# Kernel tuning notes

Measured on AMD Instinct MI355X. Metric: run time of the kernel, lower is better.

## Reference

```python
import jax, jax.numpy as jnp
import numpy as np

ALPHA = 0.1
B, T, D = 32, 1024, 384


def _build_alive(T):
    # Expert j (1-indexed) is created at time j with lifetime 2^(ctz(j)+2)+1.
    def lifetime(j):
        k = (j & -j).bit_length() - 1
        return 2 ** (k + 2) + 1

    sets = [[j for j in range(1, t + 1) if t < j + lifetime(j)]
            for t in range(1, T + 1)]
    K = max(len(s) for s in sets)
    # pad with sentinel index T (the extra never-consumed expert slot)
    idx = np.full((T, K), T, dtype=np.int32)
    mask = np.zeros((T, K), dtype=np.float32)
    for t0, s in enumerate(sets):
        for i, j in enumerate(s):
            idx[t0, i] = j - 1  # 0-indexed expert slot
            mask[t0, i] = 1.0
    return idx, mask


def setup_inputs() -> dict:
    key = jax.random.key(0)
    kx, kw, kb = jax.random.split(key, 3)
    n_exp = T + 1
    x = jax.random.normal(kx, (B, T, D), dtype=jnp.float32)
    # stand-in STULayer = Linear(D, D) per expert
    W = jax.random.normal(kw, (n_exp, D, D), dtype=jnp.float32) / np.float32(np.sqrt(D))
    b = jax.random.normal(kb, (n_exp, D), dtype=jnp.float32) * 0.02
    idx, mask = _build_alive(T)
    return {"x": x, "W": W, "b": b,
            "alive_idx": jnp.asarray(idx), "alive_mask": jnp.asarray(mask)}


def reference(x, W, b, alive_idx, alive_mask):
    Bb, Tt, Dd = x.shape
    n_exp = W.shape[0]
    # initial pool: 1 expert with weight 1
    p0 = jnp.zeros((n_exp,), x.dtype).at[0].set(1.0)
    new_idx = jnp.arange(1, Tt + 1, dtype=jnp.int32)      # slot of expert created at step t
    t_f = jnp.arange(1, Tt + 1, dtype=x.dtype)            # p[new] = 1/t

    def step(p, inp):
        x_t, idx, mask, ni, tf = inp          # x_t: [B,D]; idx,mask: [K]
        Wg = W[idx]                            # [K,D,D]
        bg = b[idx]                            # [K,D]
        outs = jnp.einsum('bd,kde->kbe', x_t, Wg) + bg[:, None, :]  # [K,B,D]
        p_a = p[idx] * mask                    # weights of alive experts
        w = p_a / jnp.sum(p_a)                 # normalized (torch keeps them pre-normalized)
        y_t = jnp.einsum('k,kbe->be', w, outs)
        # soft cross-entropy of expert outputs against x_t (ChunkedCrossEntropyLoss stand-in)
        tgt = jax.nn.softmax(x_t, axis=-1)                       # [B,D]
        logp = jax.nn.log_softmax(outs, axis=-1)                 # [K,B,D]
        loss = -jnp.mean(jnp.sum(tgt[None, :, :] * logp, axis=-1), axis=-1)  # [K]
        loss = jax.lax.stop_gradient(loss)     # torch uses .item() => detached
        # multiplicative weight update, normalize over alive set
        p_upd = p_a * jnp.exp(-ALPHA * loss) * mask
        p_upd = p_upd / jnp.sum(p_upd)
        p = p.at[idx].set(jnp.where(mask > 0, p_upd, p[idx]))
        # spawn new expert with weight 1/t (renormalization deferred to use time)
        p = p.at[ni].set(1.0 / tf)
        return p, y_t

    xs = (jnp.swapaxes(x, 0, 1), alive_idx, alive_mask, new_idx, t_f)
    _, ys = jax.lax.scan(step, p0, xs)        # ys: [T,B,D]
    return jnp.swapaxes(ys, 0, 1)
```

## Files before the change

### kernel.cpp

```cpp
#include <hip/hip_runtime.h>

#define TT 1024
#define BB 32
#define DD 384
#define NE 1025
#define ALPHA_ 0.1f
#define TC 4
#define KSTEP 64
#define NKS 6
#define MROWS 128
#define PADK 72
#define NTHR 512

typedef __attribute__((ext_vector_type(8))) short short8;
typedef __attribute__((ext_vector_type(8))) unsigned short ushort8;
typedef __attribute__((ext_vector_type(4))) float f32x4;

__device__ __forceinline__ unsigned short f2bf(float f) {
    unsigned int u = __float_as_uint(f);
    unsigned int r = u + 0x7fffu + ((u >> 16) & 1u);
    return (unsigned short)(r >> 16);
}

__device__ __host__ __forceinline__ int chunks_of(int j, int* Lout) {
    int k = __builtin_ctz(j);
    int life = (1 << (k + 2)) + 1;
    int jend = j + life - 1; if (jend > TT) jend = TT;
    int L = jend - j + 1;
    *Lout = L;
    return (L + TC - 1) / TC;
}

__device__ __forceinline__ void gl16(const void* g, void* l) {
    __builtin_amdgcn_global_load_lds(
        (const __attribute__((address_space(1))) void*)g,
        (__attribute__((address_space(3))) void*)l, 16, 0, 0);
}

__device__ __forceinline__ float dppsum32(float v) {
    float t;
    t = __int_as_float(__builtin_amdgcn_update_dpp(0, __float_as_int(v), 0x111, 0xf, 0xf, true)); v += t;
    t = __int_as_float(__builtin_amdgcn_update_dpp(0, __float_as_int(v), 0x112, 0xf, 0xf, true)); v += t;
    t = __int_as_float(__builtin_amdgcn_update_dpp(0, __float_as_int(v), 0x114, 0xf, 0xf, true)); v += t;
    t = __int_as_float(__builtin_amdgcn_update_dpp(0, __float_as_int(v), 0x118, 0xf, 0xf, true)); v += t;
    t = __int_as_float(__builtin_amdgcn_update_dpp(0, __float_as_int(v), 0x142, 0xf, 0xf, true)); v += t;
    return __int_as_float(__builtin_amdgcn_readlane(__float_as_int(v), 31));
}

__global__ void setup_all(int* __restrict__ table, int* __restrict__ pref,
                          short* __restrict__ perm16,
                          const int* __restrict__ aidx, const float* __restrict__ amask,
                          int K) {
    __shared__ int sc[1024];
    int b = blockIdx.x, t = threadIdx.x;
    if (b == 0) {
        int j = t + 1;
        int L; int nc = chunks_of(j, &L);
        int start = 0;
        for (int jp = 1; jp < j; ++jp) { int Lp; start += chunks_of(jp, &Lp); }
        for (int c = 0; c < nc; ++c) {
            int cnt = L - c * TC; if (cnt > TC) cnt = TC;
            int* e = table + 3 * (start + c);
            e[0] = j - 1;
            e[1] = (j - 1) + c * TC;
            e[2] = cnt;
        }
    } else if (b == 1) {
        int c = 0;
        for (int kk = 0; kk < K; ++kk) c += (amask[t * K + kk] > 0.f) ? 1 : 0;
        sc[t] = c;
        __syncthreads();
        for (int off = 1; off < 1024; off <<= 1) {
            int v = (t >= off) ? sc[t - off] : 0;
            __syncthreads();
            sc[t] += v;
            __syncthreads();
        }
        if (t == 0) pref[0] = 0;
        pref[t + 1] = sc[t];
    } else {
        int t0 = b - 2;
        int l = t;
        if (l < 32) {
            short enc = 63;
            if (t0 >= 1 && t0 <= TT - 1 && l < K && amask[t0 * K + l] > 0.f) {
                int sp = aidx[t0 * K + l];
                if (sp == t0) enc = (short)(-sp);
                else {
                    for (int kk = 0; kk < K; ++kk)
                        if (aidx[(t0 - 1) * K + kk] == sp) { enc = (short)kk; break; }
                }
            }
            perm16[t0 * 32 + l] = enc;
        }
    }
}

__global__ __launch_bounds__(512)
void conv_w2(const float* __restrict__ W, unsigned short* __restrict__ Wperm) {
    int db = blockIdx.x;
    int j  = blockIdx.y;
    int tid = threadIdx.x, l = tid & 63, w8 = tid >> 6;
    const float* Wj = W + (size_t)j * (DD * DD)
                        + (size_t)(db * 32 + (l >> 4) * 8) * DD + (l & 15);
#pragma unroll
    for (int it = 0; it < 3; ++it) {
        int eblk = it * 8 + w8;
        const float* src = Wj + eblk * 16;
        ushort8 h;
#pragma unroll
        for (int k = 0; k < 8; ++k) h[k] = f2bf(src[(size_t)k * DD]);
        *(ushort8*)&Wperm[(((size_t)j * 12 + db) * 24 + eblk) * 512 + l * 8] = h;
    }
}

__global__ __launch_bounds__(512)
void conv_x2(const float* __restrict__ x, unsigned short* __restrict__ xperm) {
    int t = blockIdx.x;
    int tid = threadIdx.x, l = tid & 63, w8 = tid >> 6;
#pragma unroll
    for (int it = 0; it < 3; ++it) {
        int T = it * 8 + w8;
        int bb = T / 12, db = T - bb * 12;
        const float* src = x + ((size_t)(bb * 16 + (l & 15)) * TT + t) * DD
                             + db * 32 + (l >> 4) * 8;
        float4 f0 = *(const float4*)src;
        float4 f1 = *(const float4*)(src + 4);
        ushort8 h;
        h[0] = f2bf(f0.x); h[1] = f2bf(f0.y); h[2] = f2bf(f0.z); h[3] = f2bf(f0.w);
        h[4] = f2bf(f1.x); h[5] = f2bf(f1.y); h[6] = f2bf(f1.z); h[7] = f2bf(f1.w);
        *(ushort8*)&xperm[(size_t)t * 12288 + T * 512 + l * 8] = h;
    }
}

__global__ void conv_tgt(const float* __restrict__ x, unsigned short* __restrict__ tgtbf) {
    __shared__ unsigned short sL[8 * 384];
    int tid = threadIdx.x;
    int wid = tid >> 6, lane = tid & 63;
    size_t row = (size_t)blockIdx.x * 8 + wid;
    const float* xr = x + row * DD;
    float v[6]; float m = -1e30f;
#pragma unroll
    for (int i = 0; i < 6; ++i) { v[i] = xr[lane + 64 * i]; m = fmaxf(m, v[i]); }
#pragma unroll
    for (int d = 1; d < 64; d <<= 1) m = fmaxf(m, __shfl_xor(m, d));
    float s = 0.f;
#pragma unroll
    for (int i = 0; i < 6; ++i) { v[i] = __expf(v[i] - m); s += v[i]; }
#pragma unroll
    for (int d = 1; d < 64; d <<= 1) s += __shfl_xor(s, d);
    float rz = 1.0f / s;
#pragma unroll
    for (int i = 0; i < 6; ++i) sL[wid * 384 + lane + 64 * i] = f2bf(v[i] * rz);
    __syncthreads();
    unsigned int* dst = (unsigned int*)(tgtbf + (size_t)blockIdx.x * 8 * 384);
    const unsigned int* s32 = (const unsigned int*)sL;
#pragma unroll
    for (int i = 0; i < 3; ++i) dst[i * 512 + tid] = s32[i * 512 + tid];
}

__global__ __launch_bounds__(1024)
void gemmA(const unsigned short* __restrict__ xperm,
           const unsigned short* __restrict__ Wperm,
           const float* __restrict__ bias,
           const int* __restrict__ aidx,
           const unsigned short* __restrict__ tgtbf,
           float* __restrict__ Epad,
           const int* __restrict__ table, int nblk, int K,
           const int* __restrict__ pref,
           unsigned short* __restrict__ outs)
{
    __shared__ __align__(16) unsigned short sA[2][4096];
    __shared__ __align__(16) unsigned short sB[2][12288];
    __shared__ float sRow[128];
    __shared__ int sKK[TC];
    __shared__ int sSlot[TC];

    int bid = blockIdx.x;
    int q8 = nblk >> 3, r8 = nblk & 7;
    int xcd = bid & 7, pos = bid >> 3;
    int lb = (xcd < r8 ? xcd * (q8 + 1) : r8 * (q8 + 1) + (xcd - r8) * q8) + pos;

    int s = table[3 * lb], t0s = table[3 * lb + 1], cnt = table[3 * lb + 2];

    int tid = threadIdx.x;
    int wid = tid >> 6, lane = tid & 63;
    int waveM = wid >> 2, waveN = wid & 3;
    int lc = lane & 15, lg = lane >> 4;

    int tcl[4];
#pragma unroll
    for (int tc = 0; tc < 4; ++tc) { int t = t0s + tc; tcl[tc] = t > TT - 1 ? TT - 1 : t; }

    f32x4 acc[2][6];
    f32x4 zz = {0.f, 0.f, 0.f, 0.f};
#pragma unroll
    for (int m = 0; m < 2; ++m)
#pragma unroll
        for (int n = 0; n < 6; ++n) acc[m][n] = zz;

    const size_t wbase = (size_t)s * (12 * 24 * 512);

    auto stage = [&](int buf, int ks) {
        if (wid < 8) {
            int tc = wid >> 1, bb = wid & 1;
            const unsigned short* asrc = xperm + ((size_t)tcl[tc] * 24 + bb * 12 + ks) * 512 + lane * 8;
            gl16(asrc, &sA[buf][wid * 512]);
            const unsigned short* bsrc = Wperm + wbase + ((size_t)ks * 24 + 16 + wid) * 512 + lane * 8;
            gl16(bsrc, &sB[buf][(16 + wid) * 512]);
        } else {
            int e0 = (wid - 8) * 2;
            const unsigned short* b0 = Wperm + wbase + ((size_t)ks * 24 + e0) * 512 + lane * 8;
            gl16(b0, &sB[buf][e0 * 512]);
            gl16(b0 + 512, &sB[buf][(e0 + 1) * 512]);
        }
    };

    stage(0, 0);
    stage(1, 1);
    for (int ks = 0; ks < 12; ++ks) {
        int cur = ks & 1;
        if (ks < 11) asm volatile("s_waitcnt vmcnt(2)" ::: "memory");
        else         asm volatile("s_waitcnt vmcnt(0)" ::: "memory");
        __builtin_amdgcn_s_barrier();
        __builtin_amdgcn_sched_barrier(0);
        short8 af[2], bfr[6];
#pragma unroll
        for (int mf = 0; mf < 2; ++mf)
            af[mf] = *(const short8*)&sA[cur][(waveM * 2 + mf) * 512 + lane * 8];
#pragma unroll
        for (int nf = 0; nf < 6; ++nf)
            bfr[nf] = *(const short8*)&sB[cur][(waveN * 6 + nf) * 512 + lane * 8];
#pragma unroll
        for (int mf = 0; mf < 2; ++mf)
#pragma unroll
            for (int nf = 0; nf < 6; ++nf)
                acc[mf][nf] = __builtin_amdgcn_mfma_f32_16x16x32_bf16(af[mf], bfr[nf], acc[mf][nf], 0, 0, 0);
        __builtin_amdgcn_sched_barrier(0);
        __builtin_amdgcn_s_barrier();
        __builtin_amdgcn_sched_barrier(0);
        if (ks < 10) stage(cur, ks + 2);
    }
    __syncthreads();

    float* sStat = (float*)&sA[0][0];
    if (tid < TC) {
        int kk = 0, slot = 0;
        if (tid < cnt) {
            int t = t0s + tid;
            for (int k2 = 0; k2 < K; ++k2)
                if (aidx[t * K + k2] == s) { kk = k2; break; }
            if (pref) slot = pref[t] + kk;
        }
        sKK[tid] = kk;
        sSlot[tid] = slot;
    }
#pragma unroll
    for (int nf = 0; nf < 6; ++nf) {
        float be = bias[(size_t)s * DD + waveN * 96 + nf * 16 + lc];
#pragma unroll
        for (int mf = 0; mf < 2; ++mf)
#pragma unroll
            for (int rr = 0; rr < 4; ++rr) acc[mf][nf][rr] += be;
    }
#pragma unroll
    for (int mf = 0; mf < 2; ++mf)
#pragma unroll
        for (int rr = 0; rr < 4; ++rr) {
            float m = acc[mf][0][rr];
#pragma unroll
            for (int nf = 1; nf < 6; ++nf) m = fmaxf(m, acc[mf][nf][rr]);
#pragma unroll
            for (int d = 1; d < 16; d <<= 1) m = fmaxf(m, __shfl_xor(m, d));
            if (lc == 0) sStat[(waveM * 32 + mf * 16 + lg * 4 + rr) * 12 + waveN] = m;
        }
    __syncthreads();
    if (outs && waveM < cnt) {
        unsigned short* ob = outs + (size_t)sSlot[waveM] * 12288;
#pragma unroll
        for (int mf = 0; mf < 2; ++mf)
#pragma unroll
            for (int nf = 0; nf < 6; ++nf) {
                int e = waveN * 96 + nf * 16 + lc;
#pragma unroll
                for (int rr = 0; rr < 4; ++rr) {
                    int b = mf * 16 + lg * 4 + rr;
                    ob[b * 384 + e] = f2bf(acc[mf][nf][rr]);
                }
            }
    }
#pragma unroll
    for (int mf = 0; mf < 2; ++mf)
#pragma unroll
        for (int rr = 0; rr < 4; ++rr) {
            int row = waveM * 32 + mf * 16 + lg * 4 + rr;
            const f32x4 pm = *(const f32x4*)&sStat[row * 12];
            float rmax = fmaxf(fmaxf(pm[0], pm[1]), fmaxf(pm[2], pm[3]));
            int tcr = row >> 5, b = row & 31;
            int t = tcl[tcr];
            const unsigned short* tg = tgtbf + ((size_t)b * TT + t) * DD;
            float psum = 0.f, pdot = 0.f;
#pragma unroll
            for (int nf = 0; nf < 6; ++nf) {
                int e = waveN * 96 + nf * 16 + lc;
                float a = acc[mf][nf][rr];
                psum += __expf(a - rmax);
                float tv = __uint_as_float(((unsigned int)tg[e]) << 16);
                pdot += tv * a;
            }
#pragma unroll
            for (int d = 1; d < 16; d <<= 1) { psum += __shfl_xor(psum, d); pdot += __shfl_xor(pdot, d); }
            if (lc == 0) { sStat[row * 12 + 4 + waveN] = psum; sStat[row * 12 + 8 + waveN] = pdot; }
        }
    __syncthreads();
    if (wid == 0) {
#pragma unroll
        for (int h = 0; h < 2; ++h) {
            int row = lane + h * 64;
            const f32x4 mm = *(const f32x4*)&sStat[row * 12];
            const f32x4 pp = *(const f32x4*)&sStat[row * 12 + 4];
            const f32x4 dd = *(const f32x4*)&sStat[row * 12 + 8];
            float rmax = fmaxf(fmaxf(mm[0], mm[1]), fmaxf(mm[2], mm[3]));
            float S = pp[0] + pp[1] + pp[2] + pp[3];
            float Dt = dd[0] + dd[1] + dd[2] + dd[3];
            sRow[row] = rmax + logf(S) - Dt;
        }
    }
    __syncthreads();
    if (wid == 0) {
#pragma unroll
        for (int pph = 0; pph < 2; ++pph) {
            int tc = pph * 2 + (lane >> 5);
            int b = lane & 31;
            float v = (tc < cnt) ? sRow[tc * 32 + b] : 0.f;
#pragma unroll
            for (int d = 1; d < 32; d <<= 1) v += __shfl_xor(v, d);
            if (b == 0 && tc < cnt) {
                float loss = v * (1.0f / 32.0f);
                float E = expf(-ALPHA_ * loss);
                int t0 = t0s + tc;
                Epad[t0 * 32 + sKK[tc]] = E;
            }
        }
    }
}

__global__ __launch_bounds__(256)
void recur3(const float* __restrict__ Epad, const short* __restrict__ perm16,
            const int* __restrict__ aidx, const float* __restrict__ amask,
            float* __restrict__ wraw, int K) {
    __shared__ __align__(16) float sE[2][4096];
    __shared__ __align__(16) short sP[2][4160];
    int tid = threadIdx.x, wid = tid >> 6, lane = tid & 63;
    int l = lane;

    auto stageCh = [&](int buf, int c) {
        const float* eb = Epad + c * 4096;
#pragma unroll
        for (int i = wid; i < 16; i += 4)
            gl16(eb + i * 256 + lane * 4, &sE[buf][i * 256]);
        const short* pb = perm16 + (c * 128 + 1) * 32;
#pragma unroll
        for (int i = wid; i < 8; i += 4)
            gl16(pb + i * 512 + lane * 8, &sP[buf][32 + i * 512]);
    };

    stageCh(0, 0);
    __syncthreads();

    float pr = 0.f;
    if (l < K && amask[l] > 0.f && aidx[l] == 0) pr = 1.f;

    int buf = 0;
    for (int c = 0; c < 8; ++c) {
        if (c < 7) stageCh(buf ^ 1, c + 1);
        if (wid == 0) {
            float curE = (l < 32) ? sE[buf][l] : 0.f;
            short curP = (l < 32) ? sP[buf][32 + l] : (short)63;
            for (int tl = 0; tl < 128; ++tl) {
                float nE = 0.f; short nP = 63;
                if (tl < 127) {
                    nE = sE[buf][(tl + 1) * 32 + (l & 31)];
                    nP = sP[buf][(tl + 2) * 32 + (l & 31)];
                }
                int t = c * 128 + tl;
                if (l < 32) wraw[t * 32 + l] = pr;
                float qv = pr * curE;
                float S2 = dppsum32(qv);
                float pn = qv / S2;
                int pe = (l < 32) ? (int)curP : 63;
                int src = pe >= 0 ? pe : 0;
                float sv = __shfl(pn, src);
                pr = (pe >= 0) ? sv : (1.0f / (float)(-pe));
                curE = (l < 32) ? nE : 0.f;
                curP = nP;
            }
        }
        __syncthreads();
        buf ^= 1;
    }
}

__global__ void wnorm(float* __restrict__ w) {
    int tid = threadIdx.x;
    int wid = tid >> 6, lane = tid & 63;
    int half = lane >> 5, l = lane & 31;
    int t = blockIdx.x * 8 + wid * 2 + half;
    float v = w[t * 32 + l];
    float s = v;
#pragma unroll
    for (int d = 1; d < 32; d <<= 1) s += __shfl_xor(s, d);
    w[t * 32 + l] = v / s;
}

__global__ __launch_bounds__(512)
void mixout(const unsigned short* __restrict__ outs, const float* __restrict__ wts32,
            const int* __restrict__ pref, float* __restrict__ y) {
    int t = blockIdx.x;
    __shared__ float sW[32];
    int tid = threadIdx.x;
    if (tid < 32) sW[tid] = wts32[t * 32 + tid];
    __syncthreads();
    int p0 = pref[t];
    int L = pref[t + 1] - p0;
    float acc[24];
#pragma unroll
    for (int i = 0; i < 24; ++i) acc[i] = 0.f;
    const ushort8* base = (const ushort8*)(outs + (size_t)p0 * 12288);
    for (int kk = 0; kk < L; ++kk) {
        float w = sW[kk];
        const ushort8* sp = base + (size_t)kk * 1536;
#pragma unroll
        for (int pass = 0; pass < 3; ++pass) {
            ushort8 v = sp[pass * 512 + tid];
#pragma unroll
            for (int j = 0; j < 8; ++j)
                acc[pass * 8 + j] += w * __uint_as_float(((unsigned int)v[j]) << 16);
        }
    }
#pragma unroll
    for (int pass = 0; pass < 3; ++pass) {
        int c = pass * 512 + tid;
        int b = c / 48;
        int e = (c % 48) * 8;
        float* yr = y + ((size_t)b * TT + t) * DD + e;
        float4 f0, f1;
        f0.x = acc[pass * 8 + 0]; f0.y = acc[pass * 8 + 1];
        f0.z = acc[pass * 8 + 2]; f0.w = acc[pass * 8 + 3];
        f1.x = acc[pass * 8 + 4]; f1.y = acc[pass * 8 + 5];
        f1.z = acc[pass * 8 + 6]; f1.w = acc[pass * 8 + 7];
        *(float4*)yr = f0;
        *(float4*)(yr + 4) = f1;
    }
}

__global__ void setup_blocks(int* __restrict__ table) {
    int j = threadIdx.x + 1;
    int L; int nc = chunks_of(j, &L);
    int start = 0;
    for (int jp = 1; jp < j; ++jp) { int Lp; start += chunks_of(jp, &Lp); }
    for (int c = 0; c < nc; ++c) {
        int cnt = L - c * TC; if (cnt > TC) cnt = TC;
        int* e = table + 3 * (start + c);
        e[0] = j - 1;
        e[1] = (j - 1) + c * TC;
        e[2] = cnt;
    }
}

__global__ void setup_union(int* __restrict__ uCount, int* __restrict__ uList) {
    int c = threadIdx.x;
    int t1 = 2 * c + 1, t2 = 2 * c + 2;
    int n = 0;
    for (int j = 1; j <= t2 && j <= TT; ++j) {
        int k = __builtin_ctz(j);
        int life = (1 << (k + 2)) + 1;
        if (j + life - 1 >= t1) { if (n < 32) uList[c * 32 + n] = j - 1; n++; }
    }
    uCount[c] = n > 32 ? 32 : n;
}

__global__ void setup_perm3(const int* __restrict__ aidx, const float* __restrict__ amask,
                            short* __restrict__ perm16, int K) {
    int t0 = blockIdx.x;
    int l = threadIdx.x;
    short enc = 63;
    if (t0 >= 1 && t0 <= TT - 1 && l < K && amask[t0 * K + l] > 0.f) {
        int sp = aidx[t0 * K + l];
        if (sp == t0) enc = (short)(-sp);
        else {
            for (int kk = 0; kk < K; ++kk)
                if (aidx[(t0 - 1) * K + kk] == sp) { enc = (short)kk; break; }
        }
    }
    perm16[t0 * 32 + l] = enc;
}

__global__ void conv_w(const float* __restrict__ W, unsigned short* __restrict__ Wperm) {
    int db = blockIdx.x;
    int j  = blockIdx.y;
    __shared__ __align__(16) unsigned short sL[12288];
    int tid = threadIdx.x;
    int r = tid >> 4, q = tid & 15;
    const float* src = W + (size_t)j * (DD * DD) + (size_t)(db * 32 + r) * DD + q * 24;
#pragma unroll
    for (int i = 0; i < 6; ++i) {
        float4 f = *(const float4*)(src + i * 4);
        int e0 = q * 24 + i * 4;
        float fv[4] = {f.x, f.y, f.z, f.w};
#pragma unroll
        for (int m = 0; m < 4; ++m) {
            int e = e0 + m;
            int off = (e >> 4) * 512 + (r >> 3) * 128 + (e & 15) * 8 + (r & 7);
            sL[off] = f2bf(fv[m]);
        }
    }
    __syncthreads();
    ushort8* dst = (ushort8*)(Wperm + ((size_t)j * 12 + db) * 12288);
    const ushort8* s8 = (const ushort8*)sL;
#pragma unroll
    for (int i = 0; i < 3; ++i) dst[tid * 3 + i] = s8[tid * 3 + i];
}

__global__ void conv_x(const float* __restrict__ x, unsigned short* __restrict__ xperm) {
    int t = blockIdx.x;
    __shared__ __align__(16) unsigned short sL[12288];
    int tid = threadIdx.x;
    int b = tid >> 4, q = tid & 15;
    const float* src = x + ((size_t)b * TT + t) * DD + q * 24;
#pragma unroll
    for (int i = 0; i < 6; ++i) {
        float4 f = *(const float4*)(src + i * 4);
        int d0 = q * 24 + i * 4;
        float fv[4] = {f.x, f.y, f.z, f.w};
#pragma unroll
        for (int m = 0; m < 4; ++m) {
            int d = d0 + m;
            int off = ((b >> 4) * 12 + (d >> 5)) * 512 + ((d >> 3) & 3) * 128 + (b & 15) * 8 + (d & 7);
            sL[off] = f2bf(fv[m]);
        }
    }
    __syncthreads();
    ushort8* dst = (ushort8*)(xperm + (size_t)t * 12288);
    const ushort8* s8 = (const ushort8*)sL;
#pragma unroll
    for (int i = 0; i < 3; ++i) dst[tid * 3 + i] = s8[tid * 3 + i];
}

__global__ __launch_bounds__(1024)
void gemmC(const unsigned short* __restrict__ xperm,
           const unsigned short* __restrict__ Wperm,
           const float* __restrict__ bias,
           const int* __restrict__ aidx,
           const float* __restrict__ wts32,
           const int* __restrict__ uCount, const int* __restrict__ uList,
           float* __restrict__ y, int K)
{
    __shared__ __align__(16) unsigned short sAF[24576];
    __shared__ __align__(16) unsigned short sB[2][12288];
    __shared__ float sWu[64];
    __shared__ int   sUL[32];
    __shared__ float sBv[768];

    int nb = gridDim.x;
    int bid = blockIdx.x;
    int q8 = nb >> 3, r8 = nb & 7;
    int xcd = bid & 7, pos = bid >> 3;
    int c = (xcd < r8 ? xcd * (q8 + 1) : r8 * (q8 + 1) + (xcd - r8) * q8) + pos;

    int t0 = c * 2;
    int tid = threadIdx.x, wid = tid >> 6, lane = tid & 63;
    int waveM = wid >> 2, waveN = wid & 3;
    int lc = lane & 15, lg = lane >> 4;
    int tcw = waveM >> 1, bbw = waveM & 1;

    int uc = uCount[c];
    if (tid < uc) sUL[tid] = uList[c * 32 + tid];
#pragma unroll
    for (int i = 0; i < 3; ++i) {
        int T = wid * 3 + i;
        int tc = T / 24, bb = (T / 12) & 1, db = T % 12;
        const unsigned short* src = xperm + ((size_t)(t0 + tc) * 24 + bb * 12 + db) * 512 + lane * 8;
        gl16(src, &sAF[T * 512]);
    }
    __syncthreads();
    if (tid < 2 * uc) {
        int u = tid >> 1, tc = tid & 1;
        int j = sUL[u];
        float wv = 0.f;
        for (int kk = 0; kk < K; ++kk)
            if (aidx[(t0 + tc) * K + kk] == j) { wv = wts32[(t0 + tc) * 32 + kk]; break; }
        sWu[u * 2 + tc] = wv;
    }
    __syncthreads();
    {
        size_t wb = (size_t)sUL[0] * (12 * 24 * 512);
        const unsigned short* b0 = Wperm + wb + (size_t)wid * 512 + lane * 8;
        gl16(b0, &sB[0][wid * 512]);
        if (wid < 8) {
            const unsigned short* b1 = Wperm + wb + (size_t)(16 + wid) * 512 + lane * 8;
            gl16(b1, &sB[0][(16 + wid) * 512]);
        }
    }
    for (int i = tid; i < 768; i += 1024) {
        int tc = (i >= 384) ? 1 : 0; int e = i - tc * 384;
        float a = 0.f;
        for (int u = 0; u < uc; ++u) a += sWu[u * 2 + tc] * bias[(size_t)sUL[u] * DD + e];
        sBv[i] = a;
    }
    __syncthreads();

    f32x4 accY[6], accE[6];
    f32x4 zz = {0.f, 0.f, 0.f, 0.f};
#pragma unroll
    for (int n = 0; n < 6; ++n) { accY[n] = zz; accE[n] = zz; }

    int buf = 0;
    for (int u = 0; u < uc; ++u) {
        float wv = sWu[u * 2 + tcw];
        bool act = (wv != 0.f);
        for (int ks = 0; ks < 12; ++ks) {
            int nu = u, nk = ks + 1;
            if (nk == 12) { nk = 0; nu = u + 1; }
            if (nu < uc) {
                size_t wb = (size_t)sUL[nu] * (12 * 24 * 512) + (size_t)nk * (24 * 512);
                const unsigned short* b0 = Wperm + wb + (size_t)wid * 512 + lane * 8;
                gl16(b0, &sB[buf ^ 1][wid * 512]);
                if (wid < 8) {
                    const unsigned short* b1 = Wperm + wb + (size_t)(16 + wid) * 512 + lane * 8;
                    gl16(b1, &sB[buf ^ 1][(16 + wid) * 512]);
                }
            }
            if (act) {
                short8 af = *(const short8*)&sAF[(waveM * 12 + ks) * 512 + lane * 8];
#pragma unroll
                for (int nf = 0; nf < 6; ++nf) {
                    short8 bf = *(const short8*)&sB[buf][(waveN * 6 + nf) * 512 + lane * 8];
                    accE[nf] = __builtin_amdgcn_mfma_f32_16x16x32_bf16(af, bf, accE[nf], 0, 0, 0);
                }
            }
            __syncthreads();
            buf ^= 1;
        }
        if (act) {
#pragma unroll
            for (int nf = 0; nf < 6; ++nf)
#pragma unroll
                for (int rr = 0; rr < 4; ++rr) { accY[nf][rr] += wv * accE[nf][rr]; accE[nf][rr] = 0.f; }
        }
    }

    int t = t0 + tcw;
#pragma unroll
    for (int nf = 0; nf < 6; ++nf) {
        int e = waveN * 96 + nf * 16 + lc;
        float bvv = sBv[tcw * 384 + e];
#pragma unroll
        for (int rr = 0; rr < 4; ++rr) {
            int b = bbw * 16 + lg * 4 + rr;
            y[((size_t)b * TT + t) * DD + e] = accY[nf][rr] + bvv;
        }
    }
}

__global__ void rowstats(const float* __restrict__ x, float* __restrict__ xm,
                         float* __restrict__ rz) {
    int wid = threadIdx.x >> 6;
    int lane = threadIdx.x & 63;
    int row = blockIdx.x * 4 + wid;
    const float* xr = x + (size_t)row * DD;
    float v[6];
    float m = -1e30f;
#pragma unroll
    for (int i = 0; i < 6; ++i) { v[i] = xr[lane + 64 * i]; m = fmaxf(m, v[i]); }
#pragma unroll
    for (int d = 1; d < 64; d <<= 1) m = fmaxf(m, __shfl_xor(m, d));
    float s = 0.f;
#pragma unroll
    for (int i = 0; i < 6; ++i) s += expf(v[i] - m);
#pragma unroll
    for (int d = 1; d < 64; d <<= 1) s += __shfl_xor(s, d);
    if (lane == 0) { xm[row] = m; rz[row] = 1.0f / s; }
}

template<int MODE>
__global__ __launch_bounds__(NTHR)
void gemm_phase(const float* __restrict__ x, const float* __restrict__ W,
                const float* __restrict__ bias, const int* __restrict__ aidx,
                const float* __restrict__ xm, const float* __restrict__ rz,
                const float* __restrict__ wts, float* __restrict__ Earr,
                float* __restrict__ y, const int* __restrict__ table,
                int nblk, int K)
{
    __shared__ __align__(16) unsigned short sA[MROWS * PADK];
    __shared__ __align__(16) unsigned short sB[DD * PADK];
    __shared__ float sRow[MROWS];
    __shared__ float sCoef[TC];

    int bid = blockIdx.x;
    int q = nblk >> 3, r = nblk & 7;
    int xcd = bid & 7, pos = bid >> 3;
    int lb = (xcd < r ? xcd * (q + 1) : r * (q + 1) + (xcd - r) * q) + pos;

    int s = table[3 * lb], t0s = table[3 * lb + 1], cnt = table[3 * lb + 2];

    int tid = threadIdx.x;
    int wid = tid >> 6, lane = tid & 63;
    int waveM = wid >> 2, waveN = wid & 3;
    int lc = lane & 15, lg = lane >> 4;

    if (MODE == 1 && tid < TC) {
        float c = 0.f;
        if (tid < cnt) {
            int t0 = t0s + tid;
            for (int kk = 0; kk < K; ++kk)
                if (aidx[t0 * K + kk] == s) { c = wts[t0 * K + kk]; break; }
        }
        sCoef[tid] = c;
    }

    f32x4 acc[4][6];
    f32x4 zz = {0.f, 0.f, 0.f, 0.f};
#pragma unroll
    for (int i = 0; i < 4; ++i)
#pragma unroll
        for (int n = 0; n < 6; ++n) acc[i][n] = zz;

    const float* Wj = W + (size_t)s * (DD * DD);

    int xr = tid >> 2, xq = tid & 3;
    int xtc = xr >> 5, xb = xr & 31;
    int xt = t0s + xtc; if (xt > TT - 1) xt = TT - 1;
    const float* xrow = x + ((size_t)xb * TT + xt) * DD;

    for (int ks = 0; ks < NKS; ++ks) {
        const int d0 = ks * KSTEP;
        __syncthreads();
        {
            const float4* src = (const float4*)(xrow + d0 + xq * 16);
            float4 f0 = src[0], f1 = src[1], f2 = src[2], f3 = src[3];
            short8 v0, v1;
            v0[0] = (short)f2bf(f0.x); v0[1] = (short)f2bf(f0.y);
            v0[2] = (short)f2bf(f0.z); v0[3] = (short)f2bf(f0.w);
            v0[4] = (short)f2bf(f1.x); v0[5] = (short)f2bf(f1.y);
            v0[6] = (short)f2bf(f1.z); v0[7] = (short)f2bf(f1.w);
            v1[0] = (short)f2bf(f2.x); v1[1] = (short)f2bf(f2.y);
            v1[2] = (short)f2bf(f2.z); v1[3] = (short)f2bf(f2.w);
            v1[4] = (short)f2bf(f3.x); v1[5] = (short)f2bf(f3.y);
            v1[6] = (short)f2bf(f3.z); v1[7] = (short)f2bf(f3.w);
            short8* dst = (short8*)&sA[xr * PADK + xq * 16];
            dst[0] = v0; dst[1] = v1;
        }
        {
            int dbase = d0 + wid * 8;
#pragma unroll
            for (int g = 0; g < 6; ++g) {
                int e = g * 64 + lane;
                const float* col = Wj + (size_t)dbase * DD + e;
                short8 h;
#pragma unroll
                for (int dd = 0; dd < 8; ++dd) h[dd] = (short)f2bf(col[(size_t)dd * DD]);
                *(short8*)&sB[e * PADK + wid * 8] = h;
            }
        }
        __syncthreads();
#pragma unroll
        for (int kh = 0; kh < 2; ++kh) {
            short8 af[4], bfr[6];
#pragma unroll
            for (int mf = 0; mf < 4; ++mf)
                af[mf] = *(const short8*)&sA[(waveM * 64 + mf * 16 + lc) * PADK + kh * 32 + lg * 8];
#pragma unroll
            for (int nf = 0; nf < 6; ++nf)
                bfr[nf] = *(const short8*)&sB[(waveN * 96 + nf * 16 + lc) * PADK + kh * 32 + lg * 8];
#pragma unroll
            for (int mf = 0; mf < 4; ++mf)
#pragma unroll
                for (int nf = 0; nf < 6; ++nf)
                    acc[mf][nf] = __builtin_amdgcn_mfma_f32_16x16x32_bf16(af[mf], bfr[nf], acc[mf][nf], 0, 0, 0);
        }
    }

    if (MODE == 0) {
        __syncthreads();
        float* sStat = (float*)sA;
#pragma unroll
        for (int nf = 0; nf < 6; ++nf) {
            float be = bias[(size_t)s * DD + waveN * 96 + nf * 16 + lc];
#pragma unroll
            for (int mf = 0; mf < 4; ++mf)
#pragma unroll
                for (int rr = 0; rr < 4; ++rr) acc[mf][nf][rr] += be;
        }
#pragma unroll
        for (int mf = 0; mf < 4; ++mf)
#pragma unroll
            for (int rr = 0; rr < 4; ++rr) {
                float m = acc[mf][0][rr];
#pragma unroll
                for (int nf = 1; nf < 6; ++nf) m = fmaxf(m, acc[mf][nf][rr]);
#pragma unroll
                for (int d = 1; d < 16; d <<= 1) m = fmaxf(m, __shfl_xor(m, d));
                if (lc == 0) sStat[(waveM * 64 + mf * 16 + lg * 4 + rr) * 12 + waveN] = m;
            }
        __syncthreads();
#pragma unroll
        for (int mf = 0; mf < 4; ++mf)
#pragma unroll
            for (int rr = 0; rr < 4; ++rr) {
                int row = waveM * 64 + mf * 16 + lg * 4 + rr;
                const f32x4 pm = *(const f32x4*)&sStat[row * 12];
                float rmax = fmaxf(fmaxf(pm[0], pm[1]), fmaxf(pm[2], pm[3]));
                int tc = row >> 5, b = row & 31;
                int t = t0s + tc; if (t > TT - 1) t = TT - 1;
                float xmv = xm[b * TT + t];
                float rzv = rz[b * TT + t];
                const float* x2 = x + ((size_t)b * TT + t) * DD;
                float psum = 0.f, pdot = 0.f;
#pragma unroll
                for (int nf = 0; nf < 6; ++nf) {
                    int e = waveN * 96 + nf * 16 + lc;
                    float a = acc[mf][nf][rr];
                    psum += __expf(a - rmax);
                    float tg = __expf(x2[e] - xmv) * rzv;
                    pdot += tg * a;
                }
#pragma unroll
                for (int d = 1; d < 16; d <<= 1) {
                    psum += __shfl_xor(psum, d);
                    pdot += __shfl_xor(pdot, d);
                }
                if (lc == 0) { sStat[row * 12 + 4 + waveN] = psum; sStat[row * 12 + 8 + waveN] = pdot; }
            }
        __syncthreads();
        if (wid == 0) {
#pragma unroll
            for (int h = 0; h < 2; ++h) {
                int row = lane + h * 64;
                const f32x4 mm = *(const f32x4*)&sStat[row * 12];
                const f32x4 pp = *(const f32x4*)&sStat[row * 12 + 4];
                const f32x4 dd = *(const f32x4*)&sStat[row * 12 + 8];
                float rmax = fmaxf(fmaxf(mm[0], mm[1]), fmaxf(mm[2], mm[3]));
                float S = pp[0] + pp[1] + pp[2] + pp[3];
                float Dt = dd[0] + dd[1] + dd[2] + dd[3];
                sRow[row] = rmax + logf(S) - Dt;
            }
        }
        __syncthreads();
        if (wid == 0) {
#pragma unroll
            for (int pph = 0; pph < 2; ++pph) {
                int tc = pph * 2 + (lane >> 5);
                int b = lane & 31;
                float v = (tc < cnt) ? sRow[tc * 32 + b] : 0.f;
#pragma unroll
                for (int d = 1; d < 32; d <<= 1) v += __shfl_xor(v, d);
                if (b == 0 && tc < cnt) {
                    float loss = v * (1.0f / 32.0f);
                    float E = expf(-ALPHA_ * loss);
                    int t0 = t0s + tc;
                    for (int kk = 0; kk < K; ++kk)
                        if (aidx[t0 * K + kk] == s) { Earr[t0 * K + kk] = E; break; }
                }
            }
        }
    } else {
#pragma unroll
        for (int mf = 0; mf < 4; ++mf)
#pragma unroll
            for (int rr = 0; rr < 4; ++rr) {
                int row = waveM * 64 + mf * 16 + lg * 4 + rr;
                int tc = row >> 5, b = row & 31;
                if (tc < cnt) {
                    float c = sCoef[tc];
                    int t = t0s + tc;
                    float* yr = y + ((size_t)b * TT + t) * DD + waveN * 96 + lc;
#pragma unroll
                    for (int nf = 0; nf < 6; ++nf)
                        atomicAdd(yr + nf * 16, c * acc[mf][nf][rr]);
                }
            }
    }
}

__global__ void recurrence(const int* __restrict__ aidx, const float* __restrict__ amask,
                           const float* __restrict__ Earr, float* __restrict__ wts, int K) {
    __shared__ float p[NE];
    int l = threadIdx.x;
    for (int i = l; i < NE; i += 64) p[i] = 0.f;
    __syncthreads();
    if (l == 0) p[0] = 1.f;
    __syncthreads();

    int idxv = TT; float mv = 0.f, Ev = 1.f;
    if (l < K) { idxv = aidx[l]; mv = amask[l]; Ev = Earr[l]; }

    for (int t0 = 0; t0 < TT; ++t0) {
        int idxn = TT; float mn = 0.f, En = 1.f;
        if (t0 + 1 < TT && l < K) {
            idxn = aidx[(t0 + 1) * K + l];
            mn = amask[(t0 + 1) * K + l];
            En = Earr[(t0 + 1) * K + l];
        }
        float pa = (l < K) ? p[idxv] * mv : 0.f;
        float qv = pa * Ev;
        float S1 = pa, S2 = qv;
#pragma unroll
        for (int d = 1; d < 64; d <<= 1) {
            S1 += __shfl_xor(S1, d);
            S2 += __shfl_xor(S2, d);
        }
        float w = pa / S1;
        if (l < K) wts[t0 * K + l] = w;
        float pn = qv / S2;
        __syncthreads();
        if (l < K && mv > 0.f) p[idxv] = pn;
        if (l == 0) p[t0 + 1] = 1.0f / (float)(t0 + 1);
        __syncthreads();
        idxv = idxn; mv = mn; Ev = En;
    }
}

__global__ void bias_init(const float* __restrict__ bias, const int* __restrict__ aidx,
                          const float* __restrict__ wts, float* __restrict__ y, int K) {
    int t0 = blockIdx.x;
    int e = threadIdx.x;
    float acc = 0.f;
    for (int kk = 0; kk < K; ++kk) {
        float w = wts[t0 * K + kk];
        int s = aidx[t0 * K + kk];
        acc += w * bias[(size_t)s * DD + e];
    }
    for (int b = 0; b < BB; ++b)
        y[((size_t)b * TT + t0) * DD + e] = acc;
}

extern "C" void kernel_launch(void* const* d_in, const int* in_sizes, int n_in,
                              void* d_out, int out_size, void* d_ws, size_t ws_size,
                              hipStream_t stream) {
    const float* x = (const float*)d_in[0];
    const float* W = (const float*)d_in[1];
    const float* bv = (const float*)d_in[2];
    const int* aidx = (const int*)d_in[3];
    const float* amask = (const float*)d_in[4];
    float* y = (float*)d_out;
    const int K = in_sizes[3] / TT;

    int nblk = 0, NSLOT = 0;
    for (int j = 1; j <= TT; ++j) { int L; nblk += chunks_of(j, &L); NSLOT += L; }

    size_t szW = (size_t)1024 * 294912;
    size_t szX = (size_t)1024 * 24576;
    size_t szT = (size_t)BB * TT * DD * 2;
    size_t szEp = (size_t)TT * 32 * sizeof(float);
    size_t szWt = (size_t)TT * 32 * sizeof(float);
    size_t szPm = (size_t)(TT + 1) * 32 * sizeof(short);
    size_t szTab = (size_t)6144 * 3 * sizeof(int);
    size_t szUC = 512 * sizeof(int);
    size_t szUL = 512 * 32 * sizeof(int);
    size_t szO  = (size_t)NSLOT * 12288 * 2;
    size_t szPf = (size_t)(TT + 1) * sizeof(int);
    size_t need2 = szW + szX + szT + szEp + szWt + szPm + szTab + szUC + szUL + 256;
    size_t need1 = need2 + szO + szPf;

    if (ws_size >= need1) {
        unsigned char* p = (unsigned char*)d_ws;
        unsigned short* Wperm = (unsigned short*)p; p += szW;
        unsigned short* xperm = (unsigned short*)p; p += szX;
        unsigned short* tgtb  = (unsigned short*)p; p += szT;
        float* Epad = (float*)p; p += szEp;
        float* wts32 = (float*)p; p += szWt;
        short* perm16 = (short*)p; p += szPm;
        int* table  = (int*)p;   p += szTab;
        int* uCnt   = (int*)p;   p += szUC;
        int* uLst   = (int*)p;   p += szUL;
        int* pref   = (int*)p;   p += szPf;
        unsigned short* outs = (unsigned short*)p; p += szO;

        hipLaunchKernelGGL(setup_all, dim3(TT + 3), dim3(1024), 0, stream,
                           table, pref, perm16, aidx, amask, K);
        hipLaunchKernelGGL(conv_w2, dim3(12, 1024), dim3(512), 0, stream, W, Wperm);
        hipLaunchKernelGGL(conv_x2, dim3(TT), dim3(512), 0, stream, x, xperm);
        hipLaunchKernelGGL(conv_tgt, dim3(BB * TT / 8), dim3(512), 0, stream, x, tgtb);
        hipMemsetAsync(Epad, 0, szEp, stream);
        hipLaunchKernelGGL(gemmA, dim3(nblk), dim3(1024), 0, stream,
                           xperm, Wperm, bv, aidx, tgtb, Epad, table, nblk, K, pref, outs);
        hipLaunchKernelGGL(recur3, dim3(1), dim3(256), 0, stream,
                           Epad, perm16, aidx, amask, wts32, K);
        hipLaunchKernelGGL(wnorm, dim3(TT / 8), dim3(256), 0, stream, wts32);
        hipLaunchKernelGGL(mixout, dim3(TT), dim3(512), 0, stream, outs, wts32, pref, y);
    } else if (ws_size >= need2) {
        unsigned char* p = (unsigned char*)d_ws;
        unsigned short* Wperm = (unsigned short*)p; p += szW;
        unsigned short* xperm = (unsigned short*)p; p += szX;
        unsigned short* tgtb  = (unsigned short*)p; p += szT;
        float* Epad = (float*)p; p += szEp;
        float* wts32 = (float*)p; p += szWt;
        short* perm16 = (short*)p; p += szPm;
        int* table  = (int*)p;   p += szTab;
        int* uCnt   = (int*)p;   p += szUC;
        int* uLst   = (int*)p;   p += szUL;

        hipLaunchKernelGGL(setup_blocks, dim3(1), dim3(1024), 0, stream, table);
        hipLaunchKernelGGL(setup_union, dim3(1), dim3(512), 0, stream, uCnt, uLst);
        hipLaunchKernelGGL(setup_perm3, dim3(TT + 1), dim3(32), 0, stream, aidx, amask, perm16, K);
        hipLaunchKernelGGL(conv_w, dim3(12, 1024), dim3(512), 0, stream, W, Wperm);
        hipLaunchKernelGGL(conv_x, dim3(TT), dim3(512), 0, stream, x, xperm);
        hipLaunchKernelGGL(conv_tgt, dim3(BB * TT / 8), dim3(512), 0, stream, x, tgtb);
        hipMemsetAsync(Epad, 0, szEp, stream);
        hipLaunchKernelGGL(gemmA, dim3(nblk), dim3(1024), 0, stream,
                           xperm, Wperm, bv, aidx, tgtb, Epad, table, nblk, K,
                           (const int*)nullptr, (unsigned short*)nullptr);
        hipLaunchKernelGGL(recur3, dim3(1), dim3(256), 0, stream,
                           Epad, perm16, aidx, amask, wts32, K);
        hipLaunchKernelGGL(wnorm, dim3(TT / 8), dim3(256), 0, stream, wts32);
        hipLaunchKernelGGL(gemmC, dim3(512), dim3(1024), 0, stream,
                           xperm, Wperm, bv, aidx, wts32, uCnt, uLst, y, K);
    } else {
        float* Earr = (float*)d_ws;
        float* wts = Earr + (size_t)TT * K;
        float* xm = wts + (size_t)TT * K;
        float* rz = xm + (size_t)BB * TT;
        int* table = (int*)(rz + (size_t)BB * TT);

        hipLaunchKernelGGL(setup_blocks, dim3(1), dim3(1024), 0, stream, table);
        hipLaunchKernelGGL(rowstats, dim3(BB * TT / 4), dim3(256), 0, stream, x, xm, rz);
        hipLaunchKernelGGL((gemm_phase<0>), dim3(nblk), dim3(NTHR), 0, stream,
                           x, W, bv, aidx, xm, rz, (const float*)nullptr, Earr,
                           (float*)nullptr, table, nblk, K);
        hipLaunchKernelGGL(recurrence, dim3(1), dim3(64), 0, stream, aidx, amask, Earr, wts, K);
        hipLaunchKernelGGL(bias_init, dim3(TT), dim3(DD), 0, stream, bv, aidx, wts, y, K);
        hipLaunchKernelGGL((gemm_phase<1>), dim3(nblk), dim3(NTHR), 0, stream,
                           x, W, bv, aidx, xm, rz, wts, (float*)nullptr, y, table, nblk, K);
    }
}
```

Baseline: 1.084 ms.

## Store expert outputs in MFMA fragment order with packed bf16 converts

Expert GEMM outputs are now written to the intermediate buffer in MFMA fragment-native order. Each lane packs four values with v_cvt_pk_bf16_f32 and issues one 8-byte store, replacing scattered 2-byte stores. The mixing kernel that reads this buffer is updated to decode the new layout when writing y, which now uses float2 stores. The MFMA loop is also wrapped in s_setprio to raise wave priority during compute. The aim is fewer, wider output stores, at the cost of less contiguous final y writes.

```diff
diff --git a/kernel.cpp b/kernel.cpp
--- a/kernel.cpp
+++ b/kernel.cpp
@@ -231,11 +231,13 @@
 #pragma unroll
         for (int nf = 0; nf < 6; ++nf)
             bfr[nf] = *(const short8*)&sB[cur][(waveN * 6 + nf) * 512 + lane * 8];
+        __builtin_amdgcn_s_setprio(1);
 #pragma unroll
         for (int mf = 0; mf < 2; ++mf)
 #pragma unroll
             for (int nf = 0; nf < 6; ++nf)
                 acc[mf][nf] = __builtin_amdgcn_mfma_f32_16x16x32_bf16(af[mf], bfr[nf], acc[mf][nf], 0, 0, 0);
+        __builtin_amdgcn_s_setprio(0);
         __builtin_amdgcn_sched_barrier(0);
         __builtin_amdgcn_s_barrier();
         __builtin_amdgcn_sched_barrier(0);
@@ -281,12 +283,14 @@
         for (int mf = 0; mf < 2; ++mf)
 #pragma unroll
             for (int nf = 0; nf < 6; ++nf) {
-                int e = waveN * 96 + nf * 16 + lc;
-#pragma unroll
-                for (int rr = 0; rr < 4; ++rr) {
-                    int b = mf * 16 + lg * 4 + rr;
-                    ob[b * 384 + e] = f2bf(acc[mf][nf][rr]);
-                }
+                int c2 = mf * 24 + waveN * 6 + nf;
+                unsigned int lo, hi;
+                asm("v_cvt_pk_bf16_f32 %0, %1, %2" : "=v"(lo)
+                    : "v"(acc[mf][nf][0]), "v"(acc[mf][nf][1]));
+                asm("v_cvt_pk_bf16_f32 %0, %1, %2" : "=v"(hi)
+                    : "v"(acc[mf][nf][2]), "v"(acc[mf][nf][3]));
+                uint2 pk; pk.x = lo; pk.y = hi;
+                *(uint2*)&ob[c2 * 256 + lane * 4] = pk;
             }
     }
 #pragma unroll
@@ -440,17 +444,22 @@
     }
 #pragma unroll
     for (int pass = 0; pass < 3; ++pass) {
-        int c = pass * 512 + tid;
-        int b = c / 48;
-        int e = (c % 48) * 8;
-        float* yr = y + ((size_t)b * TT + t) * DD + e;
-        float4 f0, f1;
-        f0.x = acc[pass * 8 + 0]; f0.y = acc[pass * 8 + 1];
-        f0.z = acc[pass * 8 + 2]; f0.w = acc[pass * 8 + 3];
-        f1.x = acc[pass * 8 + 4]; f1.y = acc[pass * 8 + 5];
-        f1.z = acc[pass * 8 + 6]; f1.w = acc[pass * 8 + 7];
-        *(float4*)yr = f0;
-        *(float4*)(yr + 4) = f1;
+        int idx = pass * 512 + tid;
+        int c2 = idx >> 5;
+        int lane0 = (idx * 2) & 63;
+        int mf = (c2 >= 24) ? 1 : 0;
+        int rem = c2 - mf * 24;
+        int wN = rem / 6, nf = rem - wN * 6;
+        int e0 = wN * 96 + nf * 16 + (lane0 & 15);
+        int bb = mf * 16 + (lane0 >> 4) * 4;
+#pragma unroll
+        for (int r = 0; r < 4; ++r) {
+            int b = bb + r;
+            float2 st;
+            st.x = acc[pass * 8 + r];
+            st.y = acc[pass * 8 + 4 + r];
+            *(float2*)&y[((size_t)b * TT + t) * DD + e0] = st;
+        }
     }
 }
 
```

Result: no change. 1.064 ms (-1.8%).
